# Kernel tuning notes

Hardware: AMD Instinct MI355X
Metric: run time of the kernel (lower is better)

## Reference

```python
import jax, jax.numpy as jnp
import numpy as np

DIM = 1024
N_HEAD = 16
HEAD_DIM = DIM // N_HEAD
B, T = 4, 2048
NEG = -1e9


def setup_inputs() -> dict:
    key = jax.random.key(0)
    ks = jax.random.split(key, 5)
    x = jax.random.normal(ks[0], (B, T, DIM), dtype=jnp.float32)
    # additive causal mask, broadcast over batch and heads
    causal = jnp.triu(jnp.full((T, T), NEG, dtype=jnp.float32), k=1)
    mask = causal[None, None, :, :]  # [1,1,T,T]
    s = 1.0 / np.sqrt(DIM)
    wq = jax.random.normal(ks[1], (DIM, DIM), dtype=jnp.float32) * s
    wk = jax.random.normal(ks[2], (DIM, DIM), dtype=jnp.float32) * s
    wv = jax.random.normal(ks[3], (DIM, DIM), dtype=jnp.float32) * s
    wo = jax.random.normal(ks[4], (DIM, DIM), dtype=jnp.float32) * s
    return {"x": x, "mask": mask, "wq": wq, "wk": wk, "wv": wv, "wo": wo}


def reference(x, mask, wq, wk, wv, wo):
    Bn, Tn, C = x.shape
    # torch nn.Linear(dim,dim,bias=False): y = x @ W^T
    q = (x @ wq.T).reshape(Bn, Tn, N_HEAD, HEAD_DIM).transpose(0, 2, 1, 3)  # [B,H,T,D]
    k = (x @ wk.T).reshape(Bn, Tn, N_HEAD, HEAD_DIM).transpose(0, 2, 1, 3)
    v = (x @ wv.T).reshape(Bn, Tn, N_HEAD, HEAD_DIM).transpose(0, 2, 1, 3)
    scale = 1.0 / np.sqrt(HEAD_DIM).astype(np.float32)
    attn = jnp.einsum('bhqd,bhkd->bhqk', q, k) * scale  # [B,H,T,T]
    attn = attn + mask
    attn = jax.nn.softmax(attn, axis=-1)
    out = jnp.einsum('bhqk,bhkd->bhqd', attn, v)  # [B,H,T,D]
    out = out.transpose(0, 2, 1, 3).reshape(Bn, Tn, C)
    return out @ wo.T
```

## Files before the change

### kernel.cpp

```cpp
#include <hip/hip_runtime.h>
#include <hip/hip_bf16.h>

typedef __attribute__((ext_vector_type(8))) short short8;
typedef __attribute__((ext_vector_type(4))) short short4v;
typedef __attribute__((ext_vector_type(4))) float float4v;

#define DIM   1024
#define NH    16
#define HD    64
#define BSZ   4
#define TSZ   2048
#define BT    (BSZ*TSZ)

#define SBIAS 24.0f

#define PIDX(row, col) ((((row)*64 + (col)) ^ (((row)&7) << 3)))

typedef const __attribute__((address_space(1))) void* gptr_t;
typedef __attribute__((address_space(3))) void* lptr_t;

__device__ __forceinline__ short f2bs(float x) {
    __hip_bfloat16 h = __float2bfloat16(x);
    return __builtin_bit_cast(short, h);
}

__global__ __launch_bounds__(256) void cvt_kernel(
    const float* __restrict__ x,  const float* __restrict__ wq,
    const float* __restrict__ wk, const float* __restrict__ wv,
    const float* __restrict__ wo,
    __hip_bfloat16* __restrict__ xb,  __hip_bfloat16* __restrict__ wqb,
    __hip_bfloat16* __restrict__ wkb, __hip_bfloat16* __restrict__ wvb,
    __hip_bfloat16* __restrict__ wob)
{
    int bid = blockIdx.x;
    const float* src; __hip_bfloat16* dst; int base;
    if (bid < 8192) { src = x; dst = xb; base = bid; }
    else {
        int wsel = (bid - 8192) >> 10;
        base = (bid - 8192) & 1023;
        src = (wsel == 0) ? wq : (wsel == 1) ? wk : (wsel == 2) ? wv : wo;
        dst = (wsel == 0) ? wqb : (wsel == 1) ? wkb : (wsel == 2) ? wvb : wob;
    }
    size_t off = (size_t)base * 1024 + threadIdx.x * 4;
    float4v v = *(const float4v*)(src + off);
    short4v o;
    o[0] = f2bs(v[0]); o[1] = f2bs(v[1]); o[2] = f2bs(v[2]); o[3] = f2bs(v[3]);
    *(short4v*)((short*)dst + off) = o;
}

__device__ __forceinline__ void gemm_core(
    const __hip_bfloat16* __restrict__ A,
    const __hip_bfloat16* __restrict__ B,
    __hip_bfloat16* smA, __hip_bfloat16* smB,
    int m0, int n0, int tid, float4v acc[4][4])
{
    const int wid = tid >> 6, lane = tid & 63;
    const int quad = lane >> 4, l15 = lane & 15;
    const int l7 = l15 & 7;
    const int wm = (wid >> 1) * 64, wn = (wid & 1) * 64;
    const int srow = tid >> 3;
    const int scol = ((tid & 7) ^ (srow & 7)) * 8;

    const __hip_bfloat16* gA0 = A + (size_t)(m0 + srow) * DIM + scol;
    const __hip_bfloat16* gB0 = B + (size_t)(n0 + srow) * DIM + scol;

    for (int kc = 0; kc < DIM; kc += 64) {
        __syncthreads();
#pragma unroll
        for (int j = 0; j < 4; j++) {
            __builtin_amdgcn_global_load_lds((gptr_t)(gA0 + (size_t)(j*32)*DIM + kc),
                (lptr_t)(smA + j*2048 + tid*8), 16, 0, 0);
            __builtin_amdgcn_global_load_lds((gptr_t)(gB0 + (size_t)(j*32)*DIM + kc),
                (lptr_t)(smB + j*2048 + tid*8), 16, 0, 0);
        }
        __syncthreads();

#pragma unroll
        for (int s = 0; s < 2; s++) {
            short8 a[4], b[4];
#pragma unroll
            for (int mb = 0; mb < 4; mb++)
                a[mb] = *(const short8*)(smA + (wm + mb*16 + l15)*64 + ((s*4 + quad) ^ l7)*8);
#pragma unroll
            for (int nb = 0; nb < 4; nb++)
                b[nb] = *(const short8*)(smB + (wn + nb*16 + l15)*64 + ((s*4 + quad) ^ l7)*8);
#pragma unroll
            for (int mb = 0; mb < 4; mb++)
#pragma unroll
                for (int nb = 0; nb < 4; nb++)
                    acc[mb][nb] = __builtin_amdgcn_mfma_f32_16x16x32_bf16(
                        a[mb], b[nb], acc[mb][nb], 0, 0, 0);
        }
    }
}

__global__ __launch_bounds__(256) void qkv_gemm(
    const __hip_bfloat16* __restrict__ xb,
    const __hip_bfloat16* __restrict__ wqb,
    const __hip_bfloat16* __restrict__ wkb,
    const __hip_bfloat16* __restrict__ wvb,
    __hip_bfloat16* __restrict__ Qt,
    __hip_bfloat16* __restrict__ Kb,
    __hip_bfloat16* __restrict__ Vt)
{
    __shared__ __hip_bfloat16 smA[128*64];
    __shared__ __hip_bfloat16 smB[128*64];

    const int z = blockIdx.z;
    const __hip_bfloat16* w = (z == 0) ? wqb : ((z == 1) ? wkb : wvb);
    const int tid = threadIdx.x;
    const int wid = tid >> 6, lane = tid & 63;
    const int quad = lane >> 4, l15 = lane & 15;
    const int m0 = blockIdx.x * 128, n0 = blockIdx.y * 128;
    const int wm0 = m0 + (wid >> 1) * 64;
    const int wn0 = n0 + (wid & 1) * 64;
    const float qscale = 0.1803368801111204f;

    float4v acc[4][4];
#pragma unroll
    for (int i = 0; i < 4; i++)
#pragma unroll
        for (int j = 0; j < 4; j++)
#pragma unroll
            for (int r = 0; r < 4; r++) acc[i][j][r] = 0.0f;

    gemm_core(xb, w, smA, smB, m0, n0, tid, acc);

    if (z != 1) {
        __hip_bfloat16* dst = (z == 0) ? Qt : Vt;
        const float sc = (z == 0) ? qscale : 1.0f;
        const int h = wn0 >> 6;
#pragma unroll
        for (int mb = 0; mb < 4; mb++) {
            int m = wm0 + mb*16 + quad*4;
            int bb = m >> 11, t0 = m & 2047;
#pragma unroll
            for (int nb = 0; nb < 4; nb++) {
                int d = nb*16 + l15;
                short4v pk;
                pk[0] = f2bs(acc[mb][nb][0] * sc); pk[1] = f2bs(acc[mb][nb][1] * sc);
                pk[2] = f2bs(acc[mb][nb][2] * sc); pk[3] = f2bs(acc[mb][nb][3] * sc);
                *(short4v*)(dst + (size_t)((bb*NH + h)*HD + d)*TSZ + t0) = pk;
            }
        }
    } else {
#pragma unroll
        for (int mb = 0; mb < 4; mb++)
#pragma unroll
            for (int r = 0; r < 4; r++) {
                int m = wm0 + mb*16 + quad*4 + r;
                int bb = m >> 11, t = m & 2047;
#pragma unroll
                for (int nb = 0; nb < 4; nb++) {
                    int n = wn0 + nb*16 + l15;
                    int h = n >> 6, d = n & 63;
                    Kb[(size_t)((bb*NH + h)*TSZ + t)*HD + d] =
                        __float2bfloat16(acc[mb][nb][r]);
                }
            }
    }
}

__global__ __launch_bounds__(256, 2) void attn(
    const __hip_bfloat16* __restrict__ Qt,
    const __hip_bfloat16* __restrict__ Kb,
    const __hip_bfloat16* __restrict__ Vt,
    __hip_bfloat16* __restrict__ Ob)
{
    __shared__ __hip_bfloat16 smK[64*64];
    __shared__ __hip_bfloat16 smV[64*64];
    __shared__ __hip_bfloat16 Pl[4][32*64];

    const int qperm[16] = {15,14,13,12,8,9,10,11,4,5,6,7,3,2,1,0};
    const int bh = blockIdx.x;
    const int qt = qperm[blockIdx.y];
    const int q0 = qt * 128;
    const int tid = threadIdx.x;
    const int wid = tid >> 6, lane = tid & 63;
    const int quad = lane >> 4, l15 = lane & 15;
    const int l7 = l15 & 7;
    const int q0w = q0 + wid * 32;

    const __hip_bfloat16* Qp = Qt + (size_t)bh * HD * TSZ;
    const __hip_bfloat16* Kp = Kb + (size_t)bh * TSZ * HD;
    const __hip_bfloat16* Vp = Vt + (size_t)bh * HD * TSZ;
    __hip_bfloat16* P = &Pl[wid][0];

    const int srow = tid >> 3;
    const int scol = ((tid & 7) ^ (srow & 7)) * 8;

    short8 bq[2][2];
#pragma unroll
    for (int nt = 0; nt < 2; nt++)
#pragma unroll
        for (int c = 0; c < 2; c++) {
            short8 v;
#pragma unroll
            for (int j = 0; j < 8; j++)
                v[j] = ((const short*)Qp)[(size_t)(c*32 + quad*8 + j)*TSZ
                                          + (q0w + nt*16 + l15)];
            bq[nt][c] = v;
        }

    float lsum[2] = {0.f, 0.f};
    float4v ot[4][2];
#pragma unroll
    for (int mt = 0; mt < 4; mt++)
#pragma unroll
        for (int nt = 0; nt < 2; nt++)
#pragma unroll
            for (int r = 0; r < 4; r++) ot[mt][nt][r] = 0.f;

    const int ntb = 2*qt + 2;
    for (int it = 0; it < ntb; ++it) {
        const int k0 = it * 64;

        __syncthreads();
#pragma unroll
        for (int c = 0; c < 2; c++) {
            __builtin_amdgcn_global_load_lds(
                (gptr_t)(Kp + (size_t)(k0 + srow + 32*c)*HD + scol),
                (lptr_t)(smK + tid*8 + c*2048), 16, 0, 0);
            __builtin_amdgcn_global_load_lds(
                (gptr_t)(Vp + (size_t)(srow + 32*c)*TSZ + k0 + scol),
                (lptr_t)(smV + tid*8 + c*2048), 16, 0, 0);
        }
        __syncthreads();

        if (k0 > q0w + 31) continue;

        float4v st[4][2];
#pragma unroll
        for (int mt = 0; mt < 4; mt++)
#pragma unroll
            for (int nt = 0; nt < 2; nt++)
#pragma unroll
                for (int r = 0; r < 4; r++) st[mt][nt][r] = -SBIAS;
#pragma unroll
        for (int c = 0; c < 2; c++)
#pragma unroll
            for (int mt = 0; mt < 4; mt++) {
                short8 ak = *(const short8*)(smK + (mt*16 + l15)*64 + ((c*4 + quad) ^ l7)*8);
                st[mt][0] = __builtin_amdgcn_mfma_f32_16x16x32_bf16(ak, bq[0][c], st[mt][0], 0, 0, 0);
                st[mt][1] = __builtin_amdgcn_mfma_f32_16x16x32_bf16(ak, bq[1][c], st[mt][1], 0, 0, 0);
            }

        if (k0 + 63 > q0w) {
#pragma unroll
            for (int mt = 0; mt < 4; mt++) {
                if (k0 + mt*16 + 15 > q0w) {
#pragma unroll
                    for (int nt = 0; nt < 2; nt++) {
                        int qn = q0w + nt*16 + l15;
#pragma unroll
                        for (int r = 0; r < 4; r++) {
                            int kg = k0 + mt*16 + quad*4 + r;
                            if (kg > qn) st[mt][nt][r] = -1e30f;
                        }
                    }
                }
            }
        }

#pragma unroll
        for (int nt = 0; nt < 2; nt++) {
            float rs = 0.f;
#pragma unroll
            for (int mt = 0; mt < 4; mt++) {
                float p0 = exp2f(st[mt][nt][0]);
                float p1 = exp2f(st[mt][nt][1]);
                float p2 = exp2f(st[mt][nt][2]);
                float p3 = exp2f(st[mt][nt][3]);
                rs += (p0 + p1) + (p2 + p3);
                short4v pk;
                pk[0] = f2bs(p0); pk[1] = f2bs(p1);
                pk[2] = f2bs(p2); pk[3] = f2bs(p3);
                *(short4v*)(P + PIDX(nt*16 + l15, mt*16 + quad*4)) = pk;
            }
            lsum[nt] += rs;
        }

        short8 bp[2][2];
#pragma unroll
        for (int nt = 0; nt < 2; nt++)
#pragma unroll
            for (int c2 = 0; c2 < 2; c2++)
                bp[nt][c2] = *(const short8*)(P + PIDX(nt*16 + l15, c2*32 + quad*8));

#pragma unroll
        for (int c2 = 0; c2 < 2; c2++)
#pragma unroll
            for (int mt = 0; mt < 4; mt++) {
                short8 av = *(const short8*)(smV + (mt*16 + l15)*64 + ((c2*4 + quad) ^ l7)*8);
                ot[mt][0] = __builtin_amdgcn_mfma_f32_16x16x32_bf16(av, bp[0][c2], ot[mt][0], 0, 0, 0);
                ot[mt][1] = __builtin_amdgcn_mfma_f32_16x16x32_bf16(av, bp[1][c2], ot[mt][1], 0, 0, 0);
            }
    }

    const int b = bh >> 4, h = bh & 15;
#pragma unroll
    for (int nt = 0; nt < 2; nt++) {
        float ls = lsum[nt];
        ls += __shfl_xor(ls, 16);
        ls += __shfl_xor(ls, 32);
        const float inv = 1.0f / ls;
        const int qn = q0w + nt*16 + l15;
        const size_t rowbase = (size_t)((b*TSZ + qn)*NH + h) * HD;
#pragma unroll
        for (int mt = 0; mt < 4; mt++) {
            short4v pk;
            pk[0] = f2bs(ot[mt][nt][0] * inv); pk[1] = f2bs(ot[mt][nt][1] * inv);
            pk[2] = f2bs(ot[mt][nt][2] * inv); pk[3] = f2bs(ot[mt][nt][3] * inv);
            *(short4v*)(Ob + rowbase + mt*16 + quad*4) = pk;
        }
    }
}

__global__ __launch_bounds__(256) void out_gemm(
    const __hip_bfloat16* __restrict__ A,
    const __hip_bfloat16* __restrict__ w,
    float* __restrict__ out)
{
    __shared__ __hip_bfloat16 smA[64*64];
    __shared__ __hip_bfloat16 smB[128*64];

    const int tid = threadIdx.x;
    const int wid = tid >> 6, lane = tid & 63;
    const int quad = lane >> 4, l15 = lane & 15;
    const int l7 = l15 & 7;
    const int m0 = blockIdx.x * 64, n0 = blockIdx.y * 128;
    const int wn = wid * 32;
    const int srow = tid >> 3;
    const int scol = ((tid & 7) ^ (srow & 7)) * 8;

    const __hip_bfloat16* gA0 = A + (size_t)(m0 + srow) * DIM + scol;
    const __hip_bfloat16* gB0 = w + (size_t)(n0 + srow) * DIM + scol;

    float4v acc[4][2];
#pragma unroll
    for (int i = 0; i < 4; i++)
#pragma unroll
        for (int j = 0; j < 2; j++)
#pragma unroll
            for (int r = 0; r < 4; r++) acc[i][j][r] = 0.0f;

    for (int kc = 0; kc < DIM; kc += 64) {
        __syncthreads();
#pragma unroll
        for (int j = 0; j < 2; j++)
            __builtin_amdgcn_global_load_lds((gptr_t)(gA0 + (size_t)(j*32)*DIM + kc),
                (lptr_t)(smA + j*2048 + tid*8), 16, 0, 0);
#pragma unroll
        for (int j = 0; j < 4; j++)
            __builtin_amdgcn_global_load_lds((gptr_t)(gB0 + (size_t)(j*32)*DIM + kc),
                (lptr_t)(smB + j*2048 + tid*8), 16, 0, 0);
        __syncthreads();

#pragma unroll
        for (int s = 0; s < 2; s++) {
            short8 a[4], b[2];
#pragma unroll
            for (int mb = 0; mb < 4; mb++)
                a[mb] = *(const short8*)(smA + (mb*16 + l15)*64 + ((s*4 + quad) ^ l7)*8);
#pragma unroll
            for (int nb = 0; nb < 2; nb++)
                b[nb] = *(const short8*)(smB + (wn + nb*16 + l15)*64 + ((s*4 + quad) ^ l7)*8);
#pragma unroll
            for (int mb = 0; mb < 4; mb++)
#pragma unroll
                for (int nb = 0; nb < 2; nb++)
                    acc[mb][nb] = __builtin_amdgcn_mfma_f32_16x16x32_bf16(
                        a[mb], b[nb], acc[mb][nb], 0, 0, 0);
        }
    }

#pragma unroll
    for (int mb = 0; mb < 4; mb++)
#pragma unroll
        for (int nb = 0; nb < 2; nb++)
#pragma unroll
            for (int r = 0; r < 4; r++) {
                int m = m0 + mb*16 + quad*4 + r;
                int n = n0 + wn + nb*16 + l15;
                out[(size_t)m*DIM + n] = acc[mb][nb][r];
            }
}

extern "C" void kernel_launch(void* const* d_in, const int* in_sizes, int n_in,
                              void* d_out, int out_size, void* d_ws, size_t ws_size,
                              hipStream_t stream) {
    const float* x  = (const float*)d_in[0];
    const float* wq = (const float*)d_in[2];
    const float* wk = (const float*)d_in[3];
    const float* wv = (const float*)d_in[4];
    const float* wo = (const float*)d_in[5];
    float* out = (float*)d_out;

    char* ws = (char*)d_ws;
    const size_t MB = (size_t)1024 * 1024;
    __hip_bfloat16* Qt  = (__hip_bfloat16*)(ws);
    __hip_bfloat16* Kb  = (__hip_bfloat16*)(ws + 16*MB);
    __hip_bfloat16* Vt  = (__hip_bfloat16*)(ws + 32*MB);
    __hip_bfloat16* xb  = (__hip_bfloat16*)(ws + 48*MB);
    __hip_bfloat16* Ob  = (__hip_bfloat16*)(ws + 48*MB);
    __hip_bfloat16* wqb = (__hip_bfloat16*)(ws + 64*MB);
    __hip_bfloat16* wkb = (__hip_bfloat16*)(ws + 66*MB);
    __hip_bfloat16* wvb = (__hip_bfloat16*)(ws + 68*MB);
    __hip_bfloat16* wob = (__hip_bfloat16*)(ws + 70*MB);

    dim3 blk(256);
    cvt_kernel<<<dim3(8192 + 4*1024), blk, 0, stream>>>(
        x, wq, wk, wv, wo, xb, wqb, wkb, wvb, wob);
    qkv_gemm<<<dim3(BT/128, DIM/128, 3), blk, 0, stream>>>(
        xb, wqb, wkb, wvb, Qt, Kb, Vt);
    attn<<<dim3(BSZ*NH, 16), blk, 0, stream>>>(Qt, Kb, Vt, Ob);
    out_gemm<<<dim3(BT/64, DIM/128), blk, 0, stream>>>(Ob, wob, out);
}
```

Before: 254.8 us.

## Double-buffer out_gemm LDS tiles and enlarge block tile to 128x128

The output-projection GEMM now works on a 128x128 tile per block, with each of the four waves computing a 64x64 sub-tile, instead of a 64x128 tile. It also double-buffers the A and B tiles in LDS, so the next K-chunk is loaded while MFMAs run on the current one. This aims to hide global-load latency and raise operand reuse per LDS load. In exchange it uses 64KB of LDS and more accumulator registers per block, which may lower occupancy, and it halves the grid size.

```diff
diff --git a/kernel.cpp b/kernel.cpp
--- a/kernel.cpp
+++ b/kernel.cpp
@@ -321,67 +321,82 @@
     const __hip_bfloat16* __restrict__ w,
     float* __restrict__ out)
 {
-    __shared__ __hip_bfloat16 smA[64*64];
-    __shared__ __hip_bfloat16 smB[128*64];
+    __shared__ __hip_bfloat16 smA[2][128*64];
+    __shared__ __hip_bfloat16 smB[2][128*64];
 
     const int tid = threadIdx.x;
     const int wid = tid >> 6, lane = tid & 63;
     const int quad = lane >> 4, l15 = lane & 15;
     const int l7 = l15 & 7;
-    const int m0 = blockIdx.x * 64, n0 = blockIdx.y * 128;
-    const int wn = wid * 32;
+    const int m0 = blockIdx.x * 128, n0 = blockIdx.y * 128;
+    const int wm = (wid >> 1) * 64, wn = (wid & 1) * 64;
+    const int wm0 = m0 + wm, wn0 = n0 + wn;
     const int srow = tid >> 3;
     const int scol = ((tid & 7) ^ (srow & 7)) * 8;
 
     const __hip_bfloat16* gA0 = A + (size_t)(m0 + srow) * DIM + scol;
     const __hip_bfloat16* gB0 = w + (size_t)(n0 + srow) * DIM + scol;
 
-    float4v acc[4][2];
+    float4v acc[4][4];
 #pragma unroll
     for (int i = 0; i < 4; i++)
 #pragma unroll
-        for (int j = 0; j < 2; j++)
+        for (int j = 0; j < 4; j++)
 #pragma unroll
             for (int r = 0; r < 4; r++) acc[i][j][r] = 0.0f;
 
+#pragma unroll
+    for (int j = 0; j < 4; j++) {
+        __builtin_amdgcn_global_load_lds((gptr_t)(gA0 + (size_t)(j*32)*DIM),
+            (lptr_t)(&smA[0][0] + j*2048 + tid*8), 16, 0, 0);
+        __builtin_amdgcn_global_load_lds((gptr_t)(gB0 + (size_t)(j*32)*DIM),
+            (lptr_t)(&smB[0][0] + j*2048 + tid*8), 16, 0, 0);
+    }
+
+    int cur = 0;
     for (int kc = 0; kc < DIM; kc += 64) {
         __syncthreads();
-#pragma unroll
-        for (int j = 0; j < 2; j++)
-            __builtin_amdgcn_global_load_lds((gptr_t)(gA0 + (size_t)(j*32)*DIM + kc),
-                (lptr_t)(smA + j*2048 + tid*8), 16, 0, 0);
-#pragma unroll
-        for (int j = 0; j < 4; j++)
-            __builtin_amdgcn_global_load_lds((gptr_t)(gB0 + (size_t)(j*32)*DIM + kc),
-                (lptr_t)(smB + j*2048 + tid*8), 16, 0, 0);
-        __syncthreads();
-
+
+        if (kc + 64 < DIM) {
+            const int kn = kc + 64;
+#pragma unroll
+            for (int j = 0; j < 4; j++) {
+                __builtin_amdgcn_global_load_lds((gptr_t)(gA0 + (size_t)(j*32)*DIM + kn),
+                    (lptr_t)(&smA[cur^1][0] + j*2048 + tid*8), 16, 0, 0);
+                __builtin_amdgcn_global_load_lds((gptr_t)(gB0 + (size_t)(j*32)*DIM + kn),
+                    (lptr_t)(&smB[cur^1][0] + j*2048 + tid*8), 16, 0, 0);
+            }
+        }
+
+        const __hip_bfloat16* sA = &smA[cur][0];
+        const __hip_bfloat16* sB = &smB[cur][0];
 #pragma unroll
         for (int s = 0; s < 2; s++) {
-            short8 a[4], b[2];
+            short8 a[4], b[4];
 #pragma unroll
             for (int mb = 0; mb < 4; mb++)
-                a[mb] = *(const short8*)(smA + (mb*16 + l15)*64 + ((s*4 + quad) ^ l7)*8);
-#pragma unroll
-            for (int nb = 0; nb < 2; nb++)
-                b[nb] = *(const short8*)(smB + (wn + nb*16 + l15)*64 + ((s*4 + quad) ^ l7)*8);
+                a[mb] = *(const short8*)(sA + (wm + mb*16 + l15)*64 + ((s*4 + quad) ^ l7)*8);
+#pragma unroll
+            for (int nb = 0; nb < 4; nb++)
+                b[nb] = *(const short8*)(sB + (wn + nb*16 + l15)*64 + ((s*4 + quad) ^ l7)*8);
 #pragma unroll
             for (int mb = 0; mb < 4; mb++)
 #pragma unroll
-                for (int nb = 0; nb < 2; nb++)
+                for (int nb = 0; nb < 4; nb++)
                     acc[mb][nb] = __builtin_amdgcn_mfma_f32_16x16x32_bf16(
                         a[mb], b[nb], acc[mb][nb], 0, 0, 0);
         }
+        cur ^= 1;
     }
 
 #pragma unroll
     for (int mb = 0; mb < 4; mb++)
 #pragma unroll
-        for (int nb = 0; nb < 2; nb++)
+        for (int nb = 0; nb < 4; nb++)
 #pragma unroll
             for (int r = 0; r < 4; r++) {
-                int m = m0 + mb*16 + quad*4 + r;
-                int n = n0 + wn + nb*16 + l15;
+                int m = wm0 + mb*16 + quad*4 + r;
+                int n = wn0 + nb*16 + l15;
                 out[(size_t)m*DIM + n] = acc[mb][nb][r];
             }
 }
@@ -414,5 +429,5 @@
     qkv_gemm<<<dim3(BT/128, DIM/128, 3), blk, 0, stream>>>(
         xb, wqb, wkb, wvb, Qt, Kb, Vt);
     attn<<<dim3(BSZ*NH, 16), blk, 0, stream>>>(Qt, Kb, Vt, Ob);
-    out_gemm<<<dim3(BT/64, DIM/128), blk, 0, stream>>>(Ob, wob, out);
-}
+    out_gemm<<<dim3(BT/128, DIM/128), blk, 0, stream>>>(Ob, wob, out);
+}
```

Result: faster. 249.6 us (-2.0%).
